# Optimization experiments

Measured on AMD Instinct MI355X. Metric: run time of the kernel, lower is better.

Reference implementation:

```python
import jax, jax.numpy as jnp
import numpy as np

HIDDEN = 128
HEADS = 8
HEAD_DIM = HIDDEN // HEADS
N_NODES = 100000
N_EDGES = 1600000


def setup_inputs() -> dict:
    key = jax.random.key(0)
    ks = jax.random.split(key, 12)
    s = 1.0 / np.sqrt(HIDDEN)
    inp = {
        "x": jax.random.normal(ks[0], (N_NODES, HIDDEN), dtype=jnp.float32),
        "edge_index": jax.random.randint(ks[1], (2, N_EDGES), 0, N_NODES, dtype=jnp.int32),
        "edge_emb": jax.random.normal(ks[2], (N_EDGES, HIDDEN), dtype=jnp.float32),
        "q_w": jax.random.uniform(ks[3], (HIDDEN, HIDDEN), jnp.float32, -s, s),
        "q_b": jax.random.uniform(ks[4], (HIDDEN,), jnp.float32, -s, s),
        "k_w": jax.random.uniform(ks[5], (HIDDEN, HIDDEN), jnp.float32, -s, s),
        "k_b": jax.random.uniform(ks[6], (HIDDEN,), jnp.float32, -s, s),
        "v_w": jax.random.uniform(ks[7], (HIDDEN, HIDDEN), jnp.float32, -s, s),
        "v_b": jax.random.uniform(ks[8], (HIDDEN,), jnp.float32, -s, s),
        "out_w": jax.random.uniform(ks[9], (HIDDEN, HIDDEN), jnp.float32, -s, s),
        "out_b": jax.random.uniform(ks[10], (HIDDEN,), jnp.float32, -s, s),
        "eb_w": jax.random.uniform(ks[11], (HEADS, HIDDEN), jnp.float32, -s, s),
        "eb_b": jnp.zeros((HEADS,), dtype=jnp.float32),
    }
    return inp


def reference(x, edge_index, edge_emb, q_w, q_b, k_w, k_b, v_w, v_b, out_w, out_b, eb_w, eb_b):
    n = x.shape[0]
    # node projections -> [N, H, D]
    q = (x @ q_w.T + q_b).reshape(n, HEADS, HEAD_DIM)
    k = (x @ k_w.T + k_b).reshape(n, HEADS, HEAD_DIM)
    v = (x @ v_w.T + v_b).reshape(n, HEADS, HEAD_DIM)

    row, col = edge_index[0], edge_index[1]
    # per-edge scores: [E, H]
    scores = jnp.einsum('ehd,ehd->eh', q[row], k[col]) / jnp.sqrt(jnp.float32(HEAD_DIM))
    scores = scores + edge_emb @ eb_w.T + eb_b

    # segmented softmax over incoming edges of each destination node `row`
    seg_max = jax.ops.segment_max(scores, row, num_segments=n)  # [N, H]
    exp_scores = jnp.exp(scores - seg_max[row])
    seg_sum = jax.ops.segment_sum(exp_scores, row, num_segments=n)  # [N, H]
    attn = exp_scores / (seg_sum[row] + 1e-10)  # [E, H]

    # weighted scatter-aggregation of values
    weighted_v = attn[..., None] * v[col]  # [E, H, D]
    out = jax.ops.segment_sum(weighted_v, row, num_segments=n)  # [N, H, D]
    out = out.reshape(n, HIDDEN)
    return out @ out_w.T + out_b
```

## Files before the change

kernel.cpp:

```cpp
#include <hip/hip_runtime.h>

#define HID 128
#define NH 8

typedef __attribute__((ext_vector_type(8))) short short8;
typedef __attribute__((ext_vector_type(4))) float f32x4;
typedef __attribute__((ext_vector_type(2))) float f32x2;

__device__ __forceinline__ unsigned short f2bf(float f) {
    unsigned int u = __float_as_uint(f);
    u = (u + 0x7FFF + ((u >> 16) & 1)) >> 16;
    return (unsigned short)u;
}
__device__ __forceinline__ float bf2f(unsigned short s) {
    return __uint_as_float((unsigned int)s << 16);
}
__device__ __forceinline__ unsigned int pack2bf(float lo, float hi) {
    return (unsigned int)f2bf(lo) | ((unsigned int)f2bf(hi) << 16);
}

__global__ void k_init(const float* __restrict__ qw, const float* __restrict__ kw,
                       const float* __restrict__ vw, const float* __restrict__ ow,
                       unsigned short* __restrict__ wbf,
                       const int* __restrict__ row, int E, int* __restrict__ count) {
    int bid = blockIdx.x;
    int t = threadIdx.x;
    if (bid < 64) {
        int i = bid * 256 + t;
        int idx = i * 4;
        int m = idx >> 14;
        int off = idx & 16383;
        const float* src = (m == 0) ? qw : (m == 1) ? kw : (m == 2) ? vw : ow;
        float4 v = *(const float4*)(src + off);
        ushort4 o;
        o.x = f2bf(v.x); o.y = f2bf(v.y); o.z = f2bf(v.z); o.w = f2bf(v.w);
        *(ushort4*)(wbf + idx) = o;
    } else {
        int i = (bid - 64) * 256 + t;
        int stride = (gridDim.x - 64) * 256;
        for (; i < E; i += stride) atomicAdd(&count[row[i]], 1);
    }
}

__global__ void k_scan1(const int* __restrict__ in, int total,
                        int* __restrict__ out, int* __restrict__ bsums) {
    __shared__ int sd[256];
    int t = threadIdx.x;
    int base = blockIdx.x * 1024 + t * 4;
    int v0 = (base + 0 < total) ? in[base + 0] : 0;
    int v1 = (base + 1 < total) ? in[base + 1] : 0;
    int v2 = (base + 2 < total) ? in[base + 2] : 0;
    int v3 = (base + 3 < total) ? in[base + 3] : 0;
    int s = v0 + v1 + v2 + v3;
    sd[t] = s; __syncthreads();
    for (int off = 1; off < 256; off <<= 1) {
        int xx = (t >= off) ? sd[t - off] : 0;
        __syncthreads();
        sd[t] += xx;
        __syncthreads();
    }
    int excl = sd[t] - s;
    if (t == 255) bsums[blockIdx.x] = sd[255];
    int run = excl;
    if (base + 0 < total) out[base + 0] = run; run += v0;
    if (base + 1 < total) out[base + 1] = run; run += v1;
    if (base + 2 < total) out[base + 2] = run; run += v2;
    if (base + 3 < total) out[base + 3] = run;
}

__global__ void k_scan2(int* __restrict__ bs, int nb) {
    __shared__ int sd[128];
    int t = threadIdx.x;
    int vv = (t < nb) ? bs[t] : 0;
    sd[t] = vv; __syncthreads();
    for (int off = 1; off < 128; off <<= 1) {
        int xx = (t >= off) ? sd[t - off] : 0;
        __syncthreads();
        sd[t] += xx;
        __syncthreads();
    }
    if (t < nb) bs[t] = sd[t] - vv;
}

__global__ void k_scan3(int* __restrict__ out, int total, const int* __restrict__ bs) {
    int add = bs[blockIdx.x];
    int base = blockIdx.x * 1024 + threadIdx.x * 4;
    #pragma unroll
    for (int i = 0; i < 4; ++i)
        if (base + i < total) out[base + i] += add;
}

__global__ __launch_bounds__(256) void k_fat(
    const float* __restrict__ x, const unsigned short* __restrict__ wbf,
    const float* __restrict__ qb_, const float* __restrict__ kb_, const float* __restrict__ vb_,
    unsigned short* __restrict__ qkvbf, int n, int qblocks,
    const int* __restrict__ row, const int* __restrict__ col,
    const float* __restrict__ emb, const float* __restrict__ ebw,
    const float* __restrict__ ebb, const int* __restrict__ start,
    int* __restrict__ cursor, int* __restrict__ col_sorted,
    unsigned short* __restrict__ bias_s, int E)
{
    __shared__ __align__(16) char sm[17408];
    int bid = blockIdx.x;
    int t = threadIdx.x;

    if (bid < qblocks) {
        unsigned short (*xs)[136] = (unsigned short (*)[136])sm;
        int m0 = bid * 64;
        #pragma unroll
        for (int p = 0; p < 2; ++p) {
            int f = p * 256 + t;
            int r = f >> 3;
            int c16 = (f & 7) * 16;
            int node = m0 + r;
            float4 u0 = {0,0,0,0}, u1 = {0,0,0,0}, u2 = {0,0,0,0}, u3 = {0,0,0,0};
            if (node < n) {
                const float4* px = (const float4*)(x + (size_t)node * HID + c16);
                u0 = px[0]; u1 = px[1]; u2 = px[2]; u3 = px[3];
            }
            union { unsigned short u[8]; short8 v; } a, b;
            a.u[0]=f2bf(u0.x); a.u[1]=f2bf(u0.y); a.u[2]=f2bf(u0.z); a.u[3]=f2bf(u0.w);
            a.u[4]=f2bf(u1.x); a.u[5]=f2bf(u1.y); a.u[6]=f2bf(u1.z); a.u[7]=f2bf(u1.w);
            b.u[0]=f2bf(u2.x); b.u[1]=f2bf(u2.y); b.u[2]=f2bf(u2.z); b.u[3]=f2bf(u2.w);
            b.u[4]=f2bf(u3.x); b.u[5]=f2bf(u3.y); b.u[6]=f2bf(u3.z); b.u[7]=f2bf(u3.w);
            *(short8*)&xs[r][c16]     = a.v;
            *(short8*)&xs[r][c16 + 8] = b.v;
        }
        __syncthreads();

        int w = t >> 6, l = t & 63;
        int lr = l & 15, lc = l >> 4;
        short8 afr[4];
        #pragma unroll
        for (int c = 0; c < 4; ++c)
            afr[c] = *(const short8*)&xs[w * 16 + lr][c * 32 + lc * 8];

        #pragma unroll
        for (int m = 0; m < 3; ++m) {
            const float* bias = (m == 0) ? qb_ : (m == 1) ? kb_ : vb_;
            #pragma unroll
            for (int ct = 0; ct < 8; ++ct) {
                int colg = ct * 16 + lr;
                f32x4 acc = {0.f, 0.f, 0.f, 0.f};
                const unsigned short* wrow = wbf + (size_t)m * 16384 + (size_t)colg * 128 + lc * 8;
                #pragma unroll
                for (int c = 0; c < 4; ++c) {
                    short8 bfr = *(const short8*)(wrow + c * 32);
                    acc = __builtin_amdgcn_mfma_f32_16x16x32_bf16(afr[c], bfr, acc, 0, 0, 0);
                }
                float bv = bias[colg];
                #pragma unroll
                for (int r = 0; r < 4; ++r) {
                    int node = m0 + w * 16 + lc * 4 + r;
                    if (node < n)
                        qkvbf[(size_t)node * 384 + m * 128 + colg] = f2bf(acc[r] + bv);
                }
            }
        }
    } else {
        float (*Wx)[4][8][4] = (float (*)[4][8][4])sm;
        for (int i = t; i < 1024; i += 256) {
            int j = i & 3, g = (i >> 2) & 7, c = (i >> 5) & 3, h = i >> 7;
            Wx[h][c][g][j] = ebw[h * 128 + g * 16 + c * 4 + j];
        }
        float bbr[8];
        #pragma unroll
        for (int i = 0; i < 8; ++i) bbr[i] = ebb[i];
        __syncthreads();

        int l = t & 63;
        int g = l & 7;
        int sub = l >> 3;
        int e = (bid - qblocks) * 32 + (t >> 6) * 8 + sub;
        bool act = e < E;

        float p[8] = {0.f,0.f,0.f,0.f,0.f,0.f,0.f,0.f};
        if (act) {
            const float4* pe = (const float4*)(emb + (size_t)e * HID + g * 16);
            #pragma unroll
            for (int c = 0; c < 4; ++c) {
                float4 ev = pe[c];
                #pragma unroll
                for (int h = 0; h < 8; ++h) {
                    float4 wv = *(const float4*)&Wx[h][c][g][0];
                    p[h] += ev.x*wv.x + ev.y*wv.y + ev.z*wv.z + ev.w*wv.w;
                }
            }
        }
        #pragma unroll
        for (int off = 1; off < 8; off <<= 1) {
            #pragma unroll
            for (int h = 0; h < 8; ++h) p[h] += __shfl_xor(p[h], off);
        }
        if (act && g == 0) {
            int r = row[e];
            int ps = start[r] + atomicAdd(&cursor[r], 1);
            col_sorted[ps] = col[e];
            uint4 bv;
            bv.x = pack2bf(p[0] + bbr[0], p[1] + bbr[1]);
            bv.y = pack2bf(p[2] + bbr[2], p[3] + bbr[3]);
            bv.z = pack2bf(p[4] + bbr[4], p[5] + bbr[5]);
            bv.w = pack2bf(p[6] + bbr[6], p[7] + bbr[7]);
            *(uint4*)(bias_s + (size_t)ps * 8) = bv;
        }
    }
}

__global__ __launch_bounds__(256) void k_cvtk(
    const unsigned short* __restrict__ qkvbf, unsigned char* __restrict__ kp8, int n)
{
    int i = blockIdx.x * 256 + threadIdx.x;
    int node = i >> 4;
    int c8 = (i & 15) * 8;
    if (node >= n) return;
    short8 kv = *(const short8*)(qkvbf + (size_t)node * 384 + 128 + c8);
    float f[8];
    #pragma unroll
    for (int j = 0; j < 8; ++j) f[j] = bf2f((unsigned short)kv[j]);
    unsigned int lo = 0, hi = 0;
    lo = (unsigned int)__builtin_amdgcn_cvt_pk_fp8_f32(f[0], f[1], (int)lo, false);
    lo = (unsigned int)__builtin_amdgcn_cvt_pk_fp8_f32(f[2], f[3], (int)lo, true);
    hi = (unsigned int)__builtin_amdgcn_cvt_pk_fp8_f32(f[4], f[5], (int)hi, false);
    hi = (unsigned int)__builtin_amdgcn_cvt_pk_fp8_f32(f[6], f[7], (int)hi, true);
    uint2 o; o.x = lo; o.y = hi;
    *(uint2*)(kp8 + (size_t)node * HID + c8) = o;
}

__global__ __launch_bounds__(256) void k_attn(
    const unsigned short* __restrict__ qkvbf, const unsigned char* __restrict__ kp8,
    const int* __restrict__ cols, const unsigned short* __restrict__ bias_s,
    const int* __restrict__ start, unsigned short* __restrict__ aout, int n)
{
    int node = blockIdx.x * 4 + (threadIdx.x >> 6);
    if (node >= n) return;
    int l = threadIdx.x & 63;
    int slot = l >> 3;
    int h = l & 7;
    int s0 = start[node];
    int deg = start[node + 1] - s0;

    float qf[16];
    {
        const unsigned short* qp = qkvbf + (size_t)node * 384 + h * 16;
        short8 q0 = *(const short8*)qp;
        short8 q1 = *(const short8*)(qp + 8);
        #pragma unroll
        for (int i = 0; i < 8; ++i) {
            qf[i] = bf2f((unsigned short)q0[i]);
            qf[8 + i] = bf2f((unsigned short)q1[i]);
        }
    }

    float acc[16];
    #pragma unroll
    for (int i = 0; i < 16; ++i) acc[i] = 0.f;
    float denom = 0.f;

    for (int base = 0; base < deg; base += 8) {
        int idx = base + slot;
        bool act = idx < deg;
        int sidx = s0 + (act ? idx : 0);
        int c = act ? cols[sidx] : 0;
        float eb = act ? bf2f(bias_s[(size_t)sidx * 8 + h]) : 0.f;
        uint4 kw4 = *(const uint4*)(kp8 + (size_t)c * HID + h * 16);
        const unsigned short* vp = qkvbf + (size_t)c * 384 + 256 + h * 16;
        short8 va = *(const short8*)vp;
        short8 vb = *(const short8*)(vp + 8);

        float part = 0.f;
        {
            f32x2 d0 = __builtin_amdgcn_cvt_pk_f32_fp8((int)kw4.x, false);
            f32x2 d1 = __builtin_amdgcn_cvt_pk_f32_fp8((int)kw4.x, true);
            f32x2 d2 = __builtin_amdgcn_cvt_pk_f32_fp8((int)kw4.y, false);
            f32x2 d3 = __builtin_amdgcn_cvt_pk_f32_fp8((int)kw4.y, true);
            f32x2 d4 = __builtin_amdgcn_cvt_pk_f32_fp8((int)kw4.z, false);
            f32x2 d5 = __builtin_amdgcn_cvt_pk_f32_fp8((int)kw4.z, true);
            f32x2 d6 = __builtin_amdgcn_cvt_pk_f32_fp8((int)kw4.w, false);
            f32x2 d7 = __builtin_amdgcn_cvt_pk_f32_fp8((int)kw4.w, true);
            part += qf[0]*d0[0] + qf[1]*d0[1] + qf[2]*d1[0] + qf[3]*d1[1];
            part += qf[4]*d2[0] + qf[5]*d2[1] + qf[6]*d3[0] + qf[7]*d3[1];
            part += qf[8]*d4[0] + qf[9]*d4[1] + qf[10]*d5[0] + qf[11]*d5[1];
            part += qf[12]*d6[0] + qf[13]*d6[1] + qf[14]*d7[0] + qf[15]*d7[1];
        }
        float es = act ? __expf(part * 0.25f + eb) : 0.f;
        denom += es;
        #pragma unroll
        for (int i = 0; i < 8; ++i) acc[i]     += es * bf2f((unsigned short)va[i]);
        #pragma unroll
        for (int i = 0; i < 8; ++i) acc[8 + i] += es * bf2f((unsigned short)vb[i]);
    }

    #pragma unroll
    for (int off = 8; off < 64; off <<= 1) {
        denom += __shfl_xor(denom, off);
        #pragma unroll
        for (int i = 0; i < 16; ++i) acc[i] += __shfl_xor(acc[i], off);
    }
    if (slot == 0) {
        float inv = 1.f / (denom + 1e-10f);
        uint4 o0, o1;
        o0.x = pack2bf(acc[0]*inv,  acc[1]*inv);
        o0.y = pack2bf(acc[2]*inv,  acc[3]*inv);
        o0.z = pack2bf(acc[4]*inv,  acc[5]*inv);
        o0.w = pack2bf(acc[6]*inv,  acc[7]*inv);
        o1.x = pack2bf(acc[8]*inv,  acc[9]*inv);
        o1.y = pack2bf(acc[10]*inv, acc[11]*inv);
        o1.z = pack2bf(acc[12]*inv, acc[13]*inv);
        o1.w = pack2bf(acc[14]*inv, acc[15]*inv);
        unsigned short* op = aout + (size_t)node * HID + h * 16;
        *(uint4*)op       = o0;
        *(uint4*)(op + 8) = o1;
    }
}

__global__ __launch_bounds__(256) void k_outproj_mfma(
    const unsigned short* __restrict__ aout, const unsigned short* __restrict__ wbf,
    const float* __restrict__ ob, float* __restrict__ out, int n)
{
    __shared__ unsigned short hs[64][136];
    int t = threadIdx.x;
    int m0 = blockIdx.x * 64;
    #pragma unroll
    for (int p = 0; p < 4; ++p) {
        int f = p * 256 + t;
        int r = f >> 4;
        int c8 = (f & 15) * 8;
        int node = m0 + r;
        short8 val = {0,0,0,0,0,0,0,0};
        if (node < n) val = *(const short8*)(aout + (size_t)node * HID + c8);
        *(short8*)&hs[r][c8] = val;
    }
    __syncthreads();

    int w = t >> 6, l = t & 63;
    int lr = l & 15, lc = l >> 4;
    short8 afr[4];
    #pragma unroll
    for (int c = 0; c < 4; ++c)
        afr[c] = *(const short8*)&hs[w * 16 + lr][c * 32 + lc * 8];

    #pragma unroll
    for (int ct = 0; ct < 8; ++ct) {
        int colg = ct * 16 + lr;
        f32x4 acc = {0.f, 0.f, 0.f, 0.f};
        const unsigned short* wrow = wbf + (size_t)3 * 16384 + (size_t)colg * 128 + lc * 8;
        #pragma unroll
        for (int c = 0; c < 4; ++c) {
            short8 bfr = *(const short8*)(wrow + c * 32);
            acc = __builtin_amdgcn_mfma_f32_16x16x32_bf16(afr[c], bfr, acc, 0, 0, 0);
        }
        float bv = ob[colg];
        #pragma unroll
        for (int r = 0; r < 4; ++r) {
            int node = m0 + w * 16 + lc * 4 + r;
            if (node < n)
                out[(size_t)node * HID + colg] = acc[r] + bv;
        }
    }
}

extern "C" void kernel_launch(void* const* d_in, const int* in_sizes, int n_in,
                              void* d_out, int out_size, void* d_ws, size_t ws_size,
                              hipStream_t stream) {
    const float* x   = (const float*)d_in[0];
    const int*   eix = (const int*)  d_in[1];
    const float* emb = (const float*)d_in[2];
    const float* qw  = (const float*)d_in[3];
    const float* qb  = (const float*)d_in[4];
    const float* kw  = (const float*)d_in[5];
    const float* kb  = (const float*)d_in[6];
    const float* vw  = (const float*)d_in[7];
    const float* vb  = (const float*)d_in[8];
    const float* ow  = (const float*)d_in[9];
    const float* ob  = (const float*)d_in[10];
    const float* ebw = (const float*)d_in[11];
    const float* ebb = (const float*)d_in[12];

    int n = in_sizes[0] / HID;
    int E = in_sizes[2] / HID;
    const int* row = eix;
    const int* col = eix + E;

    char* wsp = (char*)d_ws;
    auto alloc = [&](size_t bytes) -> void* {
        void* p = (void*)wsp;
        wsp += (bytes + 255) & ~(size_t)255;
        return p;
    };
    unsigned short* qkvbf = (unsigned short*)alloc((size_t)n * 384 * 2);
    unsigned char* kp8    = (unsigned char*)alloc((size_t)n * HID);
    unsigned short* wbf   = (unsigned short*)alloc((size_t)4 * 16384 * 2);
    int* col_sorted       = (int*)alloc((size_t)E * 4);
    unsigned short* bias_s= (unsigned short*)alloc((size_t)E * 8 * 2);
    unsigned short* aout  = (unsigned short*)alloc((size_t)n * HID * 2);
    int* count            = (int*)alloc((size_t)(n + 2) * 4);
    int* startp           = (int*)alloc((size_t)(n + 2) * 4);
    int* bsums            = (int*)alloc(256 * 4);
    int* cursor           = (int*)alloc((size_t)n * 4);

    hipMemsetAsync(count, 0, (size_t)(n + 1) * sizeof(int), stream);
    hipMemsetAsync(cursor, 0, (size_t)n * sizeof(int), stream);

    k_init<<<64 + 2048, 256, 0, stream>>>(qw, kw, vw, ow, wbf, row, E, count);

    int total = n + 1;
    int nb = (total + 1023) / 1024;
    k_scan1<<<nb, 256, 0, stream>>>(count, total, startp, bsums);
    k_scan2<<<1, 128, 0, stream>>>(bsums, nb);
    k_scan3<<<nb, 256, 0, stream>>>(startp, total, bsums);

    int qblocks = (n + 63) / 64;
    int eblocks = (E + 31) / 32;
    k_fat<<<qblocks + eblocks, 256, 0, stream>>>(
        x, wbf, qb, kb, vb, qkvbf, n, qblocks,
        row, col, emb, ebw, ebb, startp, cursor, col_sorted, bias_s, E);

    k_cvtk<<<(n * 16 + 255) / 256, 256, 0, stream>>>(qkvbf, kp8, n);

    k_attn<<<(n + 3) / 4, 256, 0, stream>>>(qkvbf, kp8, col_sorted, bias_s,
                                            startp, aout, n);
    k_outproj_mfma<<<(n + 63) / 64, 256, 0, stream>>>(aout, wbf, ob, (float*)d_out, n);
}
```

Measured before the change: 557.2 us.

## Prefetch next edge batch in attention loop and drop scan3 pass

```diff
diff --git a/kernel.cpp b/kernel.cpp
--- a/kernel.cpp
+++ b/kernel.cpp
@@ -82,13 +82,6 @@
     if (t < nb) bs[t] = sd[t] - vv;
 }
 
-__global__ void k_scan3(int* __restrict__ out, int total, const int* __restrict__ bs) {
-    int add = bs[blockIdx.x];
-    int base = blockIdx.x * 1024 + threadIdx.x * 4;
-    #pragma unroll
-    for (int i = 0; i < 4; ++i)
-        if (base + i < total) out[base + i] += add;
-}
 
 __global__ __launch_bounds__(256) void k_fat(
     const float* __restrict__ x, const unsigned short* __restrict__ wbf,
@@ -96,9 +89,9 @@
     unsigned short* __restrict__ qkvbf, int n, int qblocks,
     const int* __restrict__ row, const int* __restrict__ col,
     const float* __restrict__ emb, const float* __restrict__ ebw,
-    const float* __restrict__ ebb, const int* __restrict__ start,
-    int* __restrict__ cursor, int* __restrict__ col_sorted,
-    unsigned short* __restrict__ bias_s, int E)
+    const float* __restrict__ ebb, const int* __restrict__ startp,
+    const int* __restrict__ bsums, int* __restrict__ cursor,
+    int* __restrict__ col_sorted, unsigned short* __restrict__ bias_s, int E)
 {
     __shared__ __align__(16) char sm[17408];
     int bid = blockIdx.x;
@@ -194,7 +187,8 @@
         }
         if (act && g == 0) {
             int r = row[e];
-            int ps = start[r] + atomicAdd(&cursor[r], 1);
+            int sg = startp[r] + bsums[r >> 10];
+            int ps = sg + atomicAdd(&cursor[r], 1);
             col_sorted[ps] = col[e];
             uint4 bv;
             bv.x = pack2bf(p[0] + bbr[0], p[1] + bbr[1]);
@@ -229,15 +223,17 @@
 __global__ __launch_bounds__(256) void k_attn(
     const unsigned short* __restrict__ qkvbf, const unsigned char* __restrict__ kp8,
     const int* __restrict__ cols, const unsigned short* __restrict__ bias_s,
-    const int* __restrict__ start, unsigned short* __restrict__ aout, int n)
+    const int* __restrict__ startp, const int* __restrict__ bsums,
+    unsigned short* __restrict__ aout, int n, int E)
 {
     int node = blockIdx.x * 4 + (threadIdx.x >> 6);
     if (node >= n) return;
     int l = threadIdx.x & 63;
     int slot = l >> 3;
     int h = l & 7;
-    int s0 = start[node];
-    int deg = start[node + 1] - s0;
+    int s0 = startp[node] + bsums[node >> 10];
+    int s1 = startp[node + 1] + bsums[(node + 1) >> 10];
+    int deg = s1 - s0;
 
     float qf[16];
     {
@@ -256,38 +252,50 @@
     for (int i = 0; i < 16; ++i) acc[i] = 0.f;
     float denom = 0.f;
 
+    int emax = E - 1;
+    int sidx = min(s0 + slot, emax);
+    bool actC = slot < deg;
+    int c = cols[sidx];
+    float ebC = bf2f(bias_s[(size_t)sidx * 8 + h]);
+    uint4 kwC = *(const uint4*)(kp8 + (size_t)c * HID + h * 16);
+    const unsigned short* vp0 = qkvbf + (size_t)c * 384 + 256 + h * 16;
+    short8 vaC = *(const short8*)vp0;
+    short8 vbC = *(const short8*)(vp0 + 8);
+
     for (int base = 0; base < deg; base += 8) {
-        int idx = base + slot;
-        bool act = idx < deg;
-        int sidx = s0 + (act ? idx : 0);
-        int c = act ? cols[sidx] : 0;
-        float eb = act ? bf2f(bias_s[(size_t)sidx * 8 + h]) : 0.f;
-        uint4 kw4 = *(const uint4*)(kp8 + (size_t)c * HID + h * 16);
-        const unsigned short* vp = qkvbf + (size_t)c * 384 + 256 + h * 16;
-        short8 va = *(const short8*)vp;
-        short8 vb = *(const short8*)(vp + 8);
+        int idxN = base + 8 + slot;
+        bool actN = idxN < deg;
+        int sidxN = min(s0 + idxN, emax);
+        int cN = cols[sidxN];
+        float ebN = bf2f(bias_s[(size_t)sidxN * 8 + h]);
+        uint4 kwN = *(const uint4*)(kp8 + (size_t)cN * HID + h * 16);
+        const unsigned short* vpN = qkvbf + (size_t)cN * 384 + 256 + h * 16;
+        short8 vaN = *(const short8*)vpN;
+        short8 vbN = *(const short8*)(vpN + 8);
 
         float part = 0.f;
         {
-            f32x2 d0 = __builtin_amdgcn_cvt_pk_f32_fp8((int)kw4.x, false);
-            f32x2 d1 = __builtin_amdgcn_cvt_pk_f32_fp8((int)kw4.x, true);
-            f32x2 d2 = __builtin_amdgcn_cvt_pk_f32_fp8((int)kw4.y, false);
-            f32x2 d3 = __builtin_amdgcn_cvt_pk_f32_fp8((int)kw4.y, true);
-            f32x2 d4 = __builtin_amdgcn_cvt_pk_f32_fp8((int)kw4.z, false);
-            f32x2 d5 = __builtin_amdgcn_cvt_pk_f32_fp8((int)kw4.z, true);
-            f32x2 d6 = __builtin_amdgcn_cvt_pk_f32_fp8((int)kw4.w, false);
-            f32x2 d7 = __builtin_amdgcn_cvt_pk_f32_fp8((int)kw4.w, true);
+            f32x2 d0 = __builtin_amdgcn_cvt_pk_f32_fp8((int)kwC.x, false);
+            f32x2 d1 = __builtin_amdgcn_cvt_pk_f32_fp8((int)kwC.x, true);
+            f32x2 d2 = __builtin_amdgcn_cvt_pk_f32_fp8((int)kwC.y, false);
+            f32x2 d3 = __builtin_amdgcn_cvt_pk_f32_fp8((int)kwC.y, true);
+            f32x2 d4 = __builtin_amdgcn_cvt_pk_f32_fp8((int)kwC.z, false);
+            f32x2 d5 = __builtin_amdgcn_cvt_pk_f32_fp8((int)kwC.z, true);
+            f32x2 d6 = __builtin_amdgcn_cvt_pk_f32_fp8((int)kwC.w, false);
+            f32x2 d7 = __builtin_amdgcn_cvt_pk_f32_fp8((int)kwC.w, true);
             part += qf[0]*d0[0] + qf[1]*d0[1] + qf[2]*d1[0] + qf[3]*d1[1];
             part += qf[4]*d2[0] + qf[5]*d2[1] + qf[6]*d3[0] + qf[7]*d3[1];
             part += qf[8]*d4[0] + qf[9]*d4[1] + qf[10]*d5[0] + qf[11]*d5[1];
             part += qf[12]*d6[0] + qf[13]*d6[1] + qf[14]*d7[0] + qf[15]*d7[1];
         }
-        float es = act ? __expf(part * 0.25f + eb) : 0.f;
+        float es = actC ? __expf(part * 0.25f + ebC) : 0.f;
         denom += es;
         #pragma unroll
-        for (int i = 0; i < 8; ++i) acc[i]     += es * bf2f((unsigned short)va[i]);
-        #pragma unroll
-        for (int i = 0; i < 8; ++i) acc[8 + i] += es * bf2f((unsigned short)vb[i]);
+        for (int i = 0; i < 8; ++i) acc[i]     += es * bf2f((unsigned short)vaC[i]);
+        #pragma unroll
+        for (int i = 0; i < 8; ++i) acc[8 + i] += es * bf2f((unsigned short)vbC[i]);
+
+        kwC = kwN; vaC = vaN; vbC = vbN; ebC = ebN; actC = actN;
     }
 
     #pragma unroll
@@ -393,13 +401,14 @@
     int* col_sorted       = (int*)alloc((size_t)E * 4);
     unsigned short* bias_s= (unsigned short*)alloc((size_t)E * 8 * 2);
     unsigned short* aout  = (unsigned short*)alloc((size_t)n * HID * 2);
+    char* zbase           = (char*)alloc(0);
     int* count            = (int*)alloc((size_t)(n + 2) * 4);
+    int* cursor           = (int*)alloc((size_t)n * 4);
+    char* zend            = (char*)alloc(0);
     int* startp           = (int*)alloc((size_t)(n + 2) * 4);
     int* bsums            = (int*)alloc(256 * 4);
-    int* cursor           = (int*)alloc((size_t)n * 4);
-
-    hipMemsetAsync(count, 0, (size_t)(n + 1) * sizeof(int), stream);
-    hipMemsetAsync(cursor, 0, (size_t)n * sizeof(int), stream);
+
+    hipMemsetAsync(zbase, 0, (size_t)(zend - zbase), stream);
 
     k_init<<<64 + 2048, 256, 0, stream>>>(qw, kw, vw, ow, wbf, row, E, count);
 
@@ -407,17 +416,16 @@
     int nb = (total + 1023) / 1024;
     k_scan1<<<nb, 256, 0, stream>>>(count, total, startp, bsums);
     k_scan2<<<1, 128, 0, stream>>>(bsums, nb);
-    k_scan3<<<nb, 256, 0, stream>>>(startp, total, bsums);
 
     int qblocks = (n + 63) / 64;
     int eblocks = (E + 31) / 32;
     k_fat<<<qblocks + eblocks, 256, 0, stream>>>(
         x, wbf, qb, kb, vb, qkvbf, n, qblocks,
-        row, col, emb, ebw, ebb, startp, cursor, col_sorted, bias_s, E);
+        row, col, emb, ebw, ebb, startp, bsums, cursor, col_sorted, bias_s, E);
 
     k_cvtk<<<(n * 16 + 255) / 256, 256, 0, stream>>>(qkvbf, kp8, n);
 
     k_attn<<<(n + 3) / 4, 256, 0, stream>>>(qkvbf, kp8, col_sorted, bias_s,
-                                            startp, aout, n);
+                                            startp, bsums, aout, n, E);
     k_outproj_mfma<<<(n + 63) / 64, 256, 0, stream>>>(aout, wbf, ob, (float*)d_out, n);
 }
```

Result: no change. 556.2 us (-0.2%).
